# Performance work log

Hardware: AMD Instinct MI355X
Metric: run time of the kernel (lower is better)

## Reference

```python
import jax, jax.numpy as jnp
import numpy as np
from math import factorial, sqrt, pi

# ---- sizes ----
LMAX = 2; K = 32; NL = 4; NB = 8; PPOLY = 5.0; RMAX = 10.0
N = 1000; E = 8000; G = 4; XDIM = 26; MLP = 128
LS = (0, 1, 2)

# ---- real Clebsch-Gordan couplings (Racah formula + complex->real basis change) ----
def _cg_c(j1, m1, j2, m2, J, M):
    if M != m1 + m2 or J < abs(j1 - j2) or J > j1 + j2:
        return 0.0
    f = factorial
    pre = sqrt((2*J+1) * f(J+j1-j2) * f(J-j1+j2) * f(j1+j2-J) / f(j1+j2+J+1))
    pre *= sqrt(f(J+M)*f(J-M)*f(j1-m1)*f(j1+m1)*f(j2-m2)*f(j2+m2))
    s = 0.0
    for k in range(j1 + j2 - J + 1):
        d = (k, j1+j2-J-k, j1-m1-k, j2+m2-k, J-j2+m1+k, J-j1-m2+k)
        if min(d) < 0:
            continue
        den = 1.0
        for t in d:
            den *= f(t)
        s += (-1.0)**k / den
    return pre * s

def _u(l):
    U = np.zeros((2*l+1, 2*l+1), dtype=complex)
    for m in range(-l, l+1):
        i = m + l
        if m < 0:
            U[i, m+l] = 1j/sqrt(2); U[i, -m+l] = -1j*((-1.0)**m)/sqrt(2)
        elif m == 0:
            U[i, l] = 1.0
        else:
            U[i, -m+l] = 1/sqrt(2); U[i, m+l] = ((-1.0)**m)/sqrt(2)
    return U

def _real_cg(l1, l2, l3):
    Tc = np.zeros((2*l1+1, 2*l2+1, 2*l3+1), dtype=complex)
    for m1 in range(-l1, l1+1):
        for m2 in range(-l2, l2+1):
            Tc[m1+l1, m2+l2, :] = [_cg_c(l1, m1, l2, m2, l3, m3) for m3 in range(-l3, l3+1)]
    T = np.einsum('am,bn,co,mno->abc', _u(l1), _u(l2), _u(l3).conj(), Tc)
    T = T.real if np.abs(T.real).sum() >= np.abs(T.imag).sum() else T.imag
    return jnp.asarray(np.ascontiguousarray(T), dtype=jnp.float32)

CG = {}
for _l1 in LS:
    for _l2 in LS:
        for _l3 in LS:
            if abs(_l1-_l2) <= _l3 <= _l1+_l2 and (_l1+_l2+_l3) % 2 == 0:
                CG[(_l1, _l2, _l3)] = _real_cg(_l1, _l2, _l3)

CONVH = sorted(CG.keys())                 # 11 parity-allowed (l_in, l_sh, l_out) paths
CONV0 = [p for p in CONVH if p[0] == 0]   # 3 paths for first layer (Kx0e input)
NUMEL0 = len(CONV0) * K * K
NUMELH = len(CONVH) * K * K

PAIRS = {lo: [(l1, l2) for l1 in LS for l2 in LS if (l1, l2, lo) in CG] for lo in LS}
TRIPLES = {lo: [(l1, l2, L, l3) for L in LS for l3 in LS if (L, l3, lo) in CG
                for (l1, l2) in PAIRS[L]] for lo in LS}
MAXP2 = max(len(PAIRS[lo]) for lo in LS)     # 4
MAXP3 = max(len(TRIPLES[lo]) for lo in LS)   # 15
CG3 = {}
for _lo in LS:
    for (_a, _b, _L, _c) in TRIPLES[_lo]:
        CG3[(_a, _b, _L, _c, _lo)] = jnp.einsum('ijl,lmo->ijmo', CG[(_a, _b, _L)], CG[(_L, _c, _lo)])

# ---- geometry embeddings ----
def _sph(u):  # u: [E,3] unit vectors; component-normalized real SH, l=0..2
    x, y, z = u[:, 0], u[:, 1], u[:, 2]
    y0 = jnp.ones_like(x)[:, None]
    y1 = sqrt(3.0) * jnp.stack([y, z, x], -1)
    y2 = jnp.stack([sqrt(15.0)*x*y, sqrt(15.0)*y*z, sqrt(5.0)/2*(3*z*z - 1),
                    sqrt(15.0)*x*z, sqrt(15.0)/2*(x*x - y*y)], -1)
    return (y0, y1, y2)

def _radial(r):  # r: [E,1] -> [E,NB] Bessel basis * polynomial cutoff (p=5)
    n = jnp.arange(1, NB + 1, dtype=r.dtype)
    bess = sqrt(2.0 / RMAX) * jnp.sin(n * pi * r / RMAX) / r
    u = r / RMAX
    p = PPOLY
    cut = 1 - (p+1)*(p+2)/2 * u**5 + p*(p+2) * u**6 - p*(p+1)/2 * u**7
    return bess * jnp.where(u < 1.0, cut, 0.0)

# ---- tensor-product conv: per-edge MLP weights -> gather, CG tensor product, scatter-sum ----
def _conv(h, src, dst, sh, ef, w1, b1, w2, b2, paths):
    w = jax.nn.relu(ef @ w1 + b1) @ w2 + b2          # [E, weight_numel]
    nto = {lo: max(1, sum(1 for q in paths if q[2] == lo)) for lo in LS}
    msg = [jnp.zeros((src.shape[0], K, 2*lo + 1), w.dtype) for lo in LS]
    off = 0
    for (li, ls, lo) in paths:
        wp = w[:, off:off + K*K].reshape(-1, K, K); off += K * K
        t = jnp.einsum('eui,es,iso->euo', h[li][src], sh[ls], CG[(li, ls, lo)])
        msg[lo] = msg[lo] + jnp.einsum('euo,euv->evo', t, wp) / sqrt(K * nto[lo])
    return [jnp.zeros((N, K, 2*lo + 1), w.dtype).at[dst].add(msg[lo]) for lo in LS]

def _bn(h, w, b, eps=1e-5):  # e3nn-style irreps batch norm (training stats)
    out = []
    for l in LS:
        xl = h[l]
        if l == 0:
            mu = jnp.mean(xl, axis=0, keepdims=True)
            var = jnp.mean((xl - mu)**2, axis=0, keepdims=True)
            out.append((xl - mu) / jnp.sqrt(var + eps) * w[l][None, :, None] + b[None, :, None])
        else:
            n2 = jnp.mean(jnp.sum(xl * xl, -1), axis=0)  # [K]
            out.append(xl / jnp.sqrt(n2 + eps)[None, :, None] * w[l][None, :, None])
    return out

# ---- equivariant product-basis block (per-channel symmetric contractions, correlation 3) ----
def _prod(A, sc, w1, w2, w3, wlin, target_ls, use_sc):
    out = []
    for lo in target_ls:
        acc = w1[lo][None, :, None] * A[lo]
        for p, (l1, l2) in enumerate(PAIRS[lo]):
            t = jnp.einsum('nki,nkj,ijo->nko', A[l1], A[l2], CG[(l1, l2, lo)])
            acc = acc + w2[lo, p][None, :, None] * t
        for p, (l1, l2, L, l3) in enumerate(TRIPLES[lo]):
            t = jnp.einsum('nki,nkj,nkm,ijmo->nko', A[l1], A[l2], A[l3], CG3[(l1, l2, L, l3, lo)])
            acc = acc + w3[lo, p][None, :, None] * t
        y = jnp.einsum('nki,kv->nvi', acc, wlin[lo])
        if use_sc:
            y = y + sc[lo]
        out.append(y)
    return out

def _forward(x, pos, w_emb, b_emb, fc0_w1, fc0_b1, fc0_w2, fc0_b2,
             fcs_w1, fcs_b1, fcs_w2, fcs_b2, bn_w, bn_b, pw1, pw2, pw3, plin,
             edge_index, batch):
    src, dst = edge_index[0], edge_index[1]
    vec = pos[src] - pos[dst]
    r = jnp.maximum(jnp.linalg.norm(vec, axis=-1, keepdims=True), 1e-6)
    sh = _sph(vec / r)
    ef = _radial(r)
    h0 = x @ w_emb + b_emb
    h = [h0[:, :, None], jnp.zeros((N, K, 3), h0.dtype), jnp.zeros((N, K, 5), h0.dtype)]
    for i in range(NL):
        if i == 0:
            m = _conv(h, src, dst, sh, ef, fc0_w1, fc0_b1, fc0_w2, fc0_b2, CONV0)
        else:
            j = i - 1
            m = _conv(h, src, dst, sh, ef, fcs_w1[j], fcs_b1[j], fcs_w2[j], fcs_b2[j], CONVH)
        m = _bn(m, bn_w[i], bn_b[i])
        last = (i == NL - 1)
        h = _prod(m, h, pw1[i], pw2[i], pw3[i], plin[i],
                  target_ls=((0,) if last else LS), use_sc=(not last))
    node = h[0][:, :, 0]                                  # [N, K]
    graph = jax.ops.segment_sum(node, batch, num_segments=G)
    return node, graph

def setup_inputs() -> dict:
    key = jax.random.key(0)
    ks = jax.random.split(key, 16)
    rn = lambda k, sh, s: jax.random.normal(k, sh, dtype=jnp.float32) * s
    return dict(
        x=rn(ks[0], (N, XDIM), 1.0),
        pos=rn(ks[1], (N, 3), 3.0),
        edge_index=jax.random.randint(ks[2], (2, E), 0, N, dtype=jnp.int32),
        batch=jnp.sort(jax.random.randint(ks[3], (N,), 0, G, dtype=jnp.int32)),
        w_emb=rn(ks[4], (XDIM, K), 1.0/sqrt(XDIM)), b_emb=jnp.zeros((K,), jnp.float32),
        fc0_w1=rn(ks[5], (NB, MLP), 1.0/sqrt(NB)), fc0_b1=jnp.zeros((MLP,), jnp.float32),
        fc0_w2=rn(ks[6], (MLP, NUMEL0), 1.0/sqrt(MLP)), fc0_b2=jnp.zeros((NUMEL0,), jnp.float32),
        fcs_w1=rn(ks[7], (NL-1, NB, MLP), 1.0/sqrt(NB)), fcs_b1=jnp.zeros((NL-1, MLP), jnp.float32),
        fcs_w2=rn(ks[8], (NL-1, MLP, NUMELH), 1.0/sqrt(MLP)), fcs_b2=jnp.zeros((NL-1, NUMELH), jnp.float32),
        bn_w=jnp.ones((NL, 3, K), jnp.float32), bn_b=jnp.zeros((NL, K), jnp.float32),
        pw1=rn(ks[9], (NL, 3, K), 0.5),
        pw2=rn(ks[10], (NL, 3, MAXP2, K), 0.3),
        pw3=rn(ks[11], (NL, 3, MAXP3, K), 0.1),
        plin=rn(ks[12], (NL, 3, K, K), 1.0/sqrt(K)),
    )

def reference(x, pos, edge_index, batch, w_emb, b_emb, fc0_w1, fc0_b1, fc0_w2, fc0_b2,
              fcs_w1, fcs_b1, fcs_w2, fcs_b2, bn_w, bn_b, pw1, pw2, pw3, plin):
    return _forward(x, pos, w_emb, b_emb, fc0_w1, fc0_b1, fc0_w2, fc0_b2,
                    fcs_w1, fcs_b1, fcs_w2, fcs_b2, bn_w, bn_b, pw1, pw2, pw3, plin,
                    edge_index, batch)
```

## Files before the change

### kernel.cpp

```cpp
#include <hip/hip_runtime.h>
#include <hip/hip_bf16.h>
#include <math.h>

#define NE 8000
#define NN 1000
#define CAP 64
#define PLANE 256000

typedef unsigned short ushortt;
typedef __attribute__((ext_vector_type(8))) short short8;
typedef __attribute__((ext_vector_type(4))) float f32x4;

__device__ const int KEYL[11][3] = {{0,0,0},{0,1,1},{0,2,2},{1,0,1},{1,1,0},{1,1,2},{1,2,1},{2,0,2},{2,1,1},{2,2,0},{2,2,2}};
__device__ const int KEYOFF[12] = {0,1,10,35,44,53,98,143,168,213,238,363};

struct PathT { int li, ls, lo, cgoff, comp; };
__device__ const PathT PATHS[11] = {
 {0,0,0,  0, 0},{0,1,1,  1, 1},{0,2,2, 10, 4},{1,0,1, 35, 9},{1,1,0, 44,12},{1,1,2, 53,13},
 {1,2,1, 98,18},{2,0,2,143,21},{2,1,1,168,26},{2,2,0,213,29},{2,2,2,238,30}};

struct CPair { int l1,l2,cga; };
struct CTrip { int l1,l2,L,cga,l3,cgb; };
constexpr CPair cPR0[3]={{0,0,0},{1,1,44},{2,2,213}};
constexpr CPair cPR1[4]={{0,1,1},{1,0,35},{1,2,98},{2,1,168}};
constexpr CPair cPR2[4]={{0,2,10},{1,1,53},{2,0,143},{2,2,238}};
constexpr CTrip cTR0[11]={
  {0,0,0,0,0,0},{1,1,0,44,0,0},{2,2,0,213,0,0},
  {0,1,1,1,1,44},{1,0,1,35,1,44},{1,2,1,98,1,44},{2,1,1,168,1,44},
  {0,2,2,10,2,213},{1,1,2,53,2,213},{2,0,2,143,2,213},{2,2,2,238,2,213}};
constexpr CTrip cTR1[15]={
  {0,0,0,0,1,1},{1,1,0,44,1,1},{2,2,0,213,1,1},
  {0,1,1,1,0,35},{1,0,1,35,0,35},{1,2,1,98,0,35},{2,1,1,168,0,35},
  {0,1,1,1,2,98},{1,0,1,35,2,98},{1,2,1,98,2,98},{2,1,1,168,2,98},
  {0,2,2,10,1,168},{1,1,2,53,1,168},{2,0,2,143,1,168},{2,2,2,238,1,168}};
constexpr CTrip cTR2[15]={
  {0,0,0,0,2,10},{1,1,0,44,2,10},{2,2,0,213,2,10},
  {0,1,1,1,1,53},{1,0,1,35,1,53},{1,2,1,98,1,53},{2,1,1,168,1,53},
  {0,2,2,10,0,143},{1,1,2,53,0,143},{2,0,2,143,0,143},{2,2,2,238,0,143},
  {0,2,2,10,2,238},{1,1,2,53,2,238},{2,0,2,143,2,238},{2,2,2,238,2,238}};
constexpr CPair getPR(int lo,int p){ return lo==0?cPR0[p]:(lo==1?cPR1[p]:cPR2[p]); }
constexpr CTrip getTR(int lo,int p){ return lo==0?cTR0[p]:(lo==1?cTR1[p]:cTR2[p]); }
constexpr int cloff(int l){ return l==0?0:(l==1?1:4); }
constexpr int nPR(int lo){ return lo==0?3:4; }
constexpr int nTR(int lo){ return lo==0?11:15; }

template<int I> struct ic_t { static constexpr int v = I; };
template<int N, int I=0, typename F>
__device__ __forceinline__ void sfor(F&& f){
  if constexpr (I < N){ f(ic_t<I>{}); sfor<N, I+1>((F&&)f); }
}

__device__ __forceinline__ int loff_(int l){ return l==0?0:(l==1?1:4); }

__device__ __forceinline__ ushortt f2bf(float x){
  union { float f; unsigned int u; } a; a.f = x;
  unsigned int r = a.u + 0x7FFFu + ((a.u >> 16) & 1u);
  return (ushortt)(r >> 16);
}

__device__ __forceinline__ void gload_lds16(const void* g, void* lds){
  __builtin_amdgcn_global_load_lds((const __attribute__((address_space(1))) void*)g,
                                   (__attribute__((address_space(3))) void*)lds, 16, 0, 0);
}

__device__ double d_fact(int n){ double f=1.0; for(int i=2;i<=n;i++) f*=(double)i; return f; }

__device__ double d_cg(int j1,int m1,int j2,int m2,int J,int M){
  if (M != m1+m2 || J < abs(j1-j2) || J > j1+j2) return 0.0;
  double pre = sqrt((2.0*J+1.0)*d_fact(J+j1-j2)*d_fact(J-j1+j2)*d_fact(j1+j2-J)/d_fact(j1+j2+J+1));
  pre *= sqrt(d_fact(J+M)*d_fact(J-M)*d_fact(j1-m1)*d_fact(j1+m1)*d_fact(j2-m2)*d_fact(j2+m2));
  double s=0.0;
  for(int k=0;k<=j1+j2-J;k++){
    int d0=k, d1=j1+j2-J-k, d2=j1-m1-k, d3=j2+m2-k, d4=J-j2+m1+k, d5=J-j1-m2+k;
    if (d0<0||d1<0||d2<0||d3<0||d4<0||d5<0) continue;
    double den = d_fact(d0)*d_fact(d1)*d_fact(d2)*d_fact(d3)*d_fact(d4)*d_fact(d5);
    s += ((k&1)?-1.0:1.0)/den;
  }
  return pre*s;
}

__device__ void d_u(int l, int i, int j, double* re, double* im){
  int m = i - l;
  *re=0.0; *im=0.0;
  const double s2 = 0.70710678118654752440;
  double par = (m & 1) ? -1.0 : 1.0;
  if (m < 0){
    if (j == m + l)  *im += s2;
    if (j == -m + l) *im += -par*s2;
  } else if (m == 0){
    if (j == l) *re = 1.0;
  } else {
    if (j == -m + l) *re += s2;
    if (j == m + l)  *re += par*s2;
  }
}

__global__ __launch_bounds__(128) void kcg1(double* tmp){
  int key = blockIdx.x;
  int l1=KEYL[key][0], l2=KEYL[key][1], l3=KEYL[key][2];
  int n1=2*l1+1, n2=2*l2+1, n3=2*l3+1;
  int nel=n1*n2*n3;
  int t=threadIdx.x;
  if (t>=nel) return;
  int a=t/(n2*n3), b=(t/n3)%n2, c=t%n3;
  double sre=0.0, sim=0.0;
  for (int mi=0;mi<n1;mi++)
    for (int ni=0;ni<n2;ni++){
      int m3 = (mi-l1)+(ni-l2);
      int oi = m3 + l3;
      if (oi<0 || oi>=n3) continue;
      double tc = d_cg(l1,mi-l1,l2,ni-l2,l3,m3);
      if (tc==0.0) continue;
      double r1,i1,r2,i2,r3,i3;
      d_u(l1,a,mi,&r1,&i1);
      d_u(l2,b,ni,&r2,&i2);
      d_u(l3,c,oi,&r3,&i3);
      double rr = r1*r2 - i1*i2;
      double ri = r1*i2 + i1*r2;
      double fr = rr*r3 + ri*i3;
      double fi = ri*r3 - rr*i3;
      sre += fr*tc; sim += fi*tc;
    }
  tmp[(size_t)(KEYOFF[key]+t)*2]   = sre;
  tmp[(size_t)(KEYOFF[key]+t)*2+1] = sim;
}

__global__ __launch_bounds__(64) void kcg2(const double* tmp, float* cgf){
  int key=threadIdx.x;
  if (key>=11) return;
  int off=KEYOFF[key], n=KEYOFF[key+1]-off;
  double sre=0.0, sim=0.0;
  for (int i=0;i<n;i++){ sre += fabs(tmp[(size_t)(off+i)*2]); sim += fabs(tmp[(size_t)(off+i)*2+1]); }
  bool takeRe = (sre >= sim);
  for (int i=0;i<n;i++) cgf[off+i] = (float)(takeRe ? tmp[(size_t)(off+i)*2] : tmp[(size_t)(off+i)*2+1]);
}

__global__ __launch_bounds__(256) void kgeom(const float* __restrict__ pos, const int* __restrict__ ei,
                                             float* __restrict__ shb, float* __restrict__ efb){
  int e = blockIdx.x*256+threadIdx.x;
  if (e>=NE) return;
  int s=ei[e], d=ei[NE+e];
  float vx=pos[s*3]-pos[d*3], vy=pos[s*3+1]-pos[d*3+1], vz=pos[s*3+2]-pos[d*3+2];
  float r = sqrtf(vx*vx+vy*vy+vz*vz);
  r = fmaxf(r, 1e-6f);
  float inv = 1.0f/r;
  float x=vx*inv, y=vy*inv, z=vz*inv;
  float* sh = shb + (size_t)e*9;
  const float s3=1.7320508075688772f, s15=3.872983346207417f, s5h=1.118033988749895f, s15h=1.9364916731037085f;
  sh[0]=1.0f;
  sh[1]=s3*y; sh[2]=s3*z; sh[3]=s3*x;
  sh[4]=s15*x*y; sh[5]=s15*y*z; sh[6]=s5h*(3.0f*z*z-1.0f); sh[7]=s15*x*z; sh[8]=s15h*(x*x-y*y);
  float u=r*0.1f;
  float cut=0.0f;
  if (u<1.0f){ float u2=u*u; float u5=u2*u2*u; cut = 1.0f - 21.0f*u5 + 35.0f*u5*u - 15.0f*u5*u2; }
  const float c0 = 0.4472135954999579f;
  const float PIF = 3.14159265358979323846f;
  float* ef = efb + (size_t)e*8;
  for (int j=0;j<8;j++)
    ef[j] = c0*sinf((float)(j+1)*PIF*r*0.1f)*inv*cut;
}

__global__ __launch_bounds__(256) void kembed(const float* __restrict__ x, const float* __restrict__ wemb,
                                              const float* __restrict__ bemb, float* __restrict__ h){
  int idx = blockIdx.x*256+threadIdx.x;
  if (idx>=NN*32) return;
  int n=idx>>5, k=idx&31;
  float a=bemb[k];
  for (int d=0;d<26;d++) a += x[n*26+d]*wemb[d*32+k];
  float* hp = h + (size_t)n*288 + k*9;
  hp[0]=a;
  #pragma unroll
  for (int c=1;c<9;c++) hp[c]=0.0f;
}

__global__ __launch_bounds__(256) void ktrans(const float* __restrict__ fc0_w2, const float* __restrict__ fcs_w2,
                                              ushortt* __restrict__ w2t0, ushortt* __restrict__ w2tH){
  int layer = blockIdx.z;
  int numel = (layer==0) ? 3072 : 11264;
  int c0 = blockIdx.x*32;
  if (c0 >= numel) return;
  const float* src = (layer==0) ? fc0_w2 : fcs_w2 + (size_t)(layer-1)*128*11264;
  ushortt* dst = (layer==0) ? w2t0 : w2tH + (size_t)(layer-1)*11264*128;
  int k0 = blockIdx.y*32;
  __shared__ float tile[32][33];
  int t = threadIdx.x;
  #pragma unroll
  for (int it=0; it<4; it++){
    int r = (t>>5) + it*8;
    tile[r][t&31] = src[(size_t)(k0+r)*numel + c0 + (t&31)];
  }
  __syncthreads();
  #pragma unroll
  for (int it=0; it<4; it++){
    int c = (t>>5) + it*8;
    int k = t&31;
    dst[(size_t)(c0+c)*128 + k0 + k] = f2bf(tile[k][c]);
  }
}

__global__ __launch_bounds__(256) void khid2(const float* __restrict__ efb, const float* __restrict__ w1,
                                             const float* __restrict__ b1, ushortt* __restrict__ hidbf){
  int idx = blockIdx.x*256+threadIdx.x;
  if (idx >= NE*16) return;
  int e = idx>>4, q = idx&15;
  int m0 = q*8;
  float efr[8];
  const float* ef = efb + (size_t)e*8;
  #pragma unroll
  for (int j=0;j<8;j++) efr[j]=ef[j];
  ushortt out8[8];
  #pragma unroll
  for (int mm=0;mm<8;mm++){
    int m = m0+mm;
    float a = b1[m];
    #pragma unroll
    for (int j=0;j<8;j++) a = fmaf(efr[j], w1[j*128+m], a);
    out8[mm] = f2bf(a>0.0f?a:0.0f);
  }
  *(short8*)(hidbf + (size_t)e*128 + m0) = *(const short8*)out8;
}

template<int NO>
__global__ __launch_bounds__(256, (NO==1?3:2)) void kmsg5(
    const float* __restrict__ hc, const float* __restrict__ shb,
    const ushortt* __restrict__ hidbf, const ushortt* __restrict__ w2t,
    const float* __restrict__ b2, const float* __restrict__ cg,
    const int* __restrict__ src, float* __restrict__ msgp, int plist){
  int p = (plist >> (blockIdx.y*8)) & 0xFF;
  int e0 = blockIdx.x*64;
  int li=PATHS[p].li, ls=PATHS[p].ls;
  int n1=2*li+1, ns=2*ls+1;
  int lioff=loff_(li), lsoff=loff_(ls);
  int cgoff=PATHS[p].cgoff;
  int comp=PATHS[p].comp;

  __shared__ __align__(16) ushortt sB[2][64*128];
  __shared__ __align__(16) float   sT[NO*2048];
  __shared__ __align__(16) float   sB2[1024];
  __shared__ int     sSRC[64];
  float* ov  = (float*)&sB[1][0];
  float* sCP = ov;
  float* sSH = ov + 1600;

  int t = threadIdx.x;
  int w = t>>6, l = t&63;

  #pragma unroll
  for (int q=0;q<4;q++){
    int R0 = w*16 + q*4;
    int row = R0 + (l>>4);
    int ks = ((l&15)*8) ^ ((row&7)<<3);
    gload_lds16(w2t + (size_t)(p*1024 + row)*128 + ks, &sB[0][R0*128]);
  }
  short8 av[4];
  {
    const ushortt* ap = hidbf + (size_t)(e0 + w*16 + (l&15))*128 + (l>>4)*8;
    #pragma unroll
    for (int kk=0;kk<4;kk++) av[kk] = *(const short8*)(ap + kk*32);
  }
  #pragma unroll
  for (int q=0;q<4;q++) sB2[t + q*256] = b2[p*1024 + t + q*256];
  if (t < 64) sSRC[t] = src[e0+t];
  for (int idx=t; idx<64*9; idx+=256) sSH[idx] = shb[(size_t)e0*9 + idx];
  __syncthreads();

  for (int idx=t; idx<64*n1*NO; idx+=256){
    int e=idx/(n1*NO), r=idx%(n1*NO), i=r/NO, o=r%NO;
    float a=0.0f;
    for (int s=0;s<ns;s++) a += cg[cgoff + (i*ns+s)*NO+o]*sSH[e*9 + lsoff + s];
    sCP[e*25 + i*NO + o]=a;
  }
  __syncthreads();

  for (int idx=t; idx<64*32; idx+=256){
    int e = idx&63, u = idx>>6;
    const float* hp = hc + (size_t)sSRC[e]*288 + u*9 + lioff;
    float hv[5];
    #pragma unroll
    for (int i=0;i<5;i++) hv[i] = hp[i];
    #pragma unroll
    for (int o=0;o<NO;o++){
      float a=0.0f;
      #pragma unroll
      for (int i=0;i<5;i++) if (i<n1) a = fmaf(hv[i], sCP[e*25 + i*NO + o], a);
      sT[(u*NO+o)*64 + e] = a;
    }
  }
  __syncthreads();

  float macc[4][2][NO];
  #pragma unroll
  for (int r=0;r<4;r++)
    #pragma unroll
    for (int vh=0;vh<2;vh++)
      #pragma unroll
      for (int o=0;o<NO;o++) macc[r][vh][o]=0.0f;

  int e_idx = w*16 + (l>>4)*4;

  for (int c=0;c<16;c++){
    int buf = c&1;
    if (c<15){
      #pragma unroll
      for (int q=0;q<4;q++){
        int R0 = w*16 + q*4;
        int row = R0 + (l>>4);
        int ks = ((l&15)*8) ^ ((row&7)<<3);
        gload_lds16(w2t + (size_t)(p*1024 + (c+1)*64 + row)*128 + ks, &sB[buf^1][R0*128]);
      }
    }
    f32x4 acc[4];
    #pragma unroll
    for (int fn=0;fn<4;fn++)
      #pragma unroll
      for (int r=0;r<4;r++) acc[fn][r]=0.0f;
    __builtin_amdgcn_s_setprio(1);
    #pragma unroll
    for (int kk=0; kk<4; kk++){
      #pragma unroll
      for (int fn=0; fn<4; fn++){
        int brow = fn*16 + (l&15);
        int kb = (kk*32 + (l>>4)*8) ^ ((brow&7)<<3);
        short8 bv = *(const short8*)&sB[buf][brow*128 + kb];
        acc[fn] = __builtin_amdgcn_mfma_f32_16x16x32_bf16(av[kk], bv, acc[fn], 0,0,0);
      }
    }
    __builtin_amdgcn_s_setprio(0);
    #pragma unroll
    for (int uu=0;uu<2;uu++){
      int ug = c*2 + uu;
      f32x4 tv[NO];
      #pragma unroll
      for (int o=0;o<NO;o++) tv[o] = *(const f32x4*)&sT[(ug*NO+o)*64 + e_idx];
      #pragma unroll
      for (int vh=0;vh<2;vh++){
        int fn = uu*2+vh;
        float b2v = sB2[c*64 + fn*16 + (l&15)];
        #pragma unroll
        for (int r=0;r<4;r++){
          float Cv = acc[fn][r] + b2v;
          #pragma unroll
          for (int o=0;o<NO;o++) macc[r][vh][o] = fmaf(Cv, tv[o][r], macc[r][vh][o]);
        }
      }
    }
    __syncthreads();
  }

  float* sW = sT;
  #pragma unroll
  for (int r=0;r<4;r++){
    int e = e_idx + r;
    #pragma unroll
    for (int vh=0;vh<2;vh++){
      int v = vh*16 + (l&15);
      int g = v>>2;
      int addr = e*32 + (((g ^ (e&7)))<<2) + (v&3);
      #pragma unroll
      for (int o=0;o<NO;o++)
        sW[o*2048 + addr] = macc[r][vh][o];
    }
  }
  __syncthreads();
  for (int j=t; j<NO*512; j+=256){
    int o = j>>9, q = j&511;
    int e = q>>3, gl = q&7;
    f32x4 vv = *(const f32x4*)&sW[o*2048 + e*32 + ((gl^(e&7))<<2)];
    *(f32x4*)(msgp + (size_t)(comp+o)*PLANE + (size_t)e0*32 + q*4) = vv;
  }
}

__global__ __launch_bounds__(320) void kbuild(const int* __restrict__ dst, int* __restrict__ cnt, int* __restrict__ lst){
  int n = blockIdx.x;
  int t = threadIdx.x;
  __shared__ int s_dstl[NE];
  __shared__ int s_cnt[321];
  for (int idx=t; idx<NE; idx+=320) s_dstl[idx]=dst[idx];
  __syncthreads();
  const int per = NE/320;
  int start=t*per, end=start+per;
  int c=0;
  for (int e=start;e<end;++e) if (s_dstl[e]==n) c++;
  s_cnt[t+1]=c;
  if (t==0) s_cnt[0]=0;
  __syncthreads();
  if (t==0){ for (int i=1;i<=320;i++) s_cnt[i]+=s_cnt[i-1]; }
  __syncthreads();
  int pos = s_cnt[t];
  for (int e=start;e<end;++e) if (s_dstl[e]==n){ if (pos<CAP) lst[n*CAP+pos]=e; pos++; }
  if (t==0){ int M=s_cnt[320]; cnt[n]=(M<CAP)?M:CAP; }
}

__global__ __launch_bounds__(320) void kgather2(const float* __restrict__ msgp, const int* __restrict__ cnt,
                                                const int* __restrict__ lst, float* __restrict__ mbuf, int full){
  int n = blockIdx.x;
  int t = threadIdx.x;
  if (t >= 288) return;
  int M = cnt[n];
  int jc = t>>5, k = t&31;
  float acc=0.0f;
  if (full){
    int pl0,pl1,pl2,pl3,np;
    if (jc==0){ pl0=0; pl1=12; pl2=29; pl3=0; np=3; }
    else if (jc<4){ int o=jc-1; pl0=1+o; pl1=9+o; pl2=18+o; pl3=26+o; np=4; }
    else { int o=jc-4; pl0=4+o; pl1=13+o; pl2=21+o; pl3=30+o; np=4; }
    for (int m=0;m<M;++m){
      int e = lst[n*CAP+m];
      int base = e*32 + k;
      float a = msgp[(size_t)pl0*PLANE + base] + msgp[(size_t)pl1*PLANE + base] + msgp[(size_t)pl2*PLANE + base];
      if (np==4) a += msgp[(size_t)pl3*PLANE + base];
      acc += a;
    }
  } else {
    for (int m=0;m<M;++m){
      int e = lst[n*CAP+m];
      acc += msgp[(size_t)jc*PLANE + e*32 + k];
    }
  }
  float norm = full ? (jc==0 ? 0.10206207261596577f : 0.08838834764831845f) : 0.17677669529663687f;
  mbuf[(size_t)n*288 + k*9 + jc] = acc*norm;
}

__global__ __launch_bounds__(256) void kbn(const float* __restrict__ mbuf, float* __restrict__ stats){
  int k = blockIdx.x, t = threadIdx.x;
  float s0=0,sq0=0,sq1=0,sq2=0;
  for (int n=t;n<NN;n+=256){
    const float* mp = mbuf + (size_t)n*288 + k*9;
    float v0=mp[0]; s0+=v0; sq0+=v0*v0;
    float a=mp[1],b=mp[2],c=mp[3]; sq1+=a*a+b*b+c*c;
    float d=mp[4],e=mp[5],f=mp[6],g=mp[7],h=mp[8]; sq2+=d*d+e*e+f*f+g*g+h*h;
  }
  __shared__ float r[4][256];
  r[0][t]=s0; r[1][t]=sq0; r[2][t]=sq1; r[3][t]=sq2;
  __syncthreads();
  for (int s=128;s>0;s>>=1){
    if (t<s){ r[0][t]+=r[0][t+s]; r[1][t]+=r[1][t+s]; r[2][t]+=r[2][t+s]; r[3][t]+=r[3][t+s]; }
    __syncthreads();
  }
  if (t==0){
    float mu = r[0][0]/(float)NN;
    float var = r[1][0]/(float)NN - mu*mu;
    stats[k]      = mu;
    stats[32+k]   = rsqrtf(var + 1e-5f);
    stats[64+k]   = rsqrtf(r[2][0]/(float)NN + 1e-5f);
    stats[96+k]   = rsqrtf(r[3][0]/(float)NN + 1e-5f);
  }
}

template<int CGA,int NA,int AO,int NB,int BO,int NO>
__device__ __forceinline__ void c2u(const float* __restrict__ cg, const float (&A)[9], const float (&B)[9], float (&out)[5]){
  #pragma unroll
  for (int o=0;o<NO;o++) out[o]=0.0f;
  #pragma unroll
  for (int i=0;i<NA;i++){
    #pragma unroll
    for (int j=0;j<NB;j++){
      float ab=A[AO+i]*B[BO+j];
      #pragma unroll
      for (int o=0;o<NO;o++) out[o]=fmaf(ab, cg[CGA+(i*NB+j)*NO+o], out[o]);
    }
  }
}
template<int CGA,int NA,int NB,int BO,int NO>
__device__ __forceinline__ void c2u5(const float* __restrict__ cg, const float (&Bb)[5], const float (&A)[9], float (&out)[5]){
  #pragma unroll
  for (int o=0;o<NO;o++) out[o]=0.0f;
  #pragma unroll
  for (int i=0;i<NA;i++){
    #pragma unroll
    for (int j=0;j<NB;j++){
      float ab=Bb[i]*A[BO+j];
      #pragma unroll
      for (int o=0;o<NO;o++) out[o]=fmaf(ab, cg[CGA+(i*NB+j)*NO+o], out[o]);
    }
  }
}

template<int LO>
__device__ __forceinline__ void do_lo(const float* __restrict__ cg, const float (&A)[9], float (&L)[9],
                                      const float* __restrict__ w1, const float* __restrict__ w2,
                                      const float* __restrict__ w3, int k){
  constexpr int NO=2*LO+1, AO=cloff(LO);
  float acc[5];
  float wc = w1[LO*32+k];
  #pragma unroll
  for (int o=0;o<NO;o++) acc[o]=wc*A[AO+o];
  sfor<nPR(LO)>([&](auto pc){
    constexpr int p = decltype(pc)::v;
    constexpr CPair P = getPR(LO,p);
    float tt[5];
    c2u<P.cga, 2*P.l1+1, cloff(P.l1), 2*P.l2+1, cloff(P.l2), NO>(cg, A, A, tt);
    float w = w2[(LO*4+p)*32+k];
    #pragma unroll
    for (int o=0;o<NO;o++) acc[o]=fmaf(w, tt[o], acc[o]);
  });
  sfor<nTR(LO)>([&](auto pc){
    constexpr int p = decltype(pc)::v;
    constexpr CTrip T = getTR(LO,p);
    constexpr int NL=2*T.L+1;
    float bb[5];
    c2u<T.cga, 2*T.l1+1, cloff(T.l1), 2*T.l2+1, cloff(T.l2), NL>(cg, A, A, bb);
    float tt[5];
    c2u5<T.cgb, NL, 2*T.l3+1, cloff(T.l3), NO>(cg, bb, A, tt);
    float w = w3[(LO*15+p)*32+k];
    #pragma unroll
    for (int o=0;o<NO;o++) acc[o]=fmaf(w, tt[o], acc[o]);
  });
  #pragma unroll
  for (int o=0;o<NO;o++) L[AO+o]=acc[o];
}

template<int LAST>
__global__ __launch_bounds__(256) void kprod3(const float* __restrict__ mbuf, const float* __restrict__ stats,
    const float* __restrict__ hc, float* __restrict__ hn,
    const float* __restrict__ bnw, const float* __restrict__ bnb,
    const float* __restrict__ w1, const float* __restrict__ w2, const float* __restrict__ w3,
    const float* __restrict__ plin, const float* __restrict__ cg, float* __restrict__ nodeout){
  int t = threadIdx.x;
  int nl = t>>5, k = t&31;
  int n = blockIdx.x*8 + nl;
  __shared__ float sL[8][32][9];
  float A[9], L[9];
  #pragma unroll
  for (int j=0;j<9;j++) L[j]=0.0f;
  const float* mp = mbuf + (size_t)n*288 + k*9;
  {
    float a0 = (mp[0]-stats[k])*stats[32+k]*bnw[k] + bnb[k];
    float f1 = stats[64+k]*bnw[32+k];
    float f2 = stats[96+k]*bnw[64+k];
    A[0]=a0;
    A[1]=mp[1]*f1; A[2]=mp[2]*f1; A[3]=mp[3]*f1;
    #pragma unroll
    for (int c=0;c<5;c++) A[4+c]=mp[4+c]*f2;
  }
  do_lo<0>(cg, A, L, w1, w2, w3, k);
  if constexpr (!LAST){
    do_lo<1>(cg, A, L, w1, w2, w3, k);
    do_lo<2>(cg, A, L, w1, w2, w3, k);
  }
  #pragma unroll
  for (int j=0;j<9;j++) sL[nl][k][j]=L[j];
  __syncthreads();

  if constexpr (!LAST){
    for (int idx=t; idx<8*288; idx+=256){
      int n2 = idx/288;
      int r  = idx%288;
      int jc = r>>5, v = r&31;
      int lo = (jc==0)?0:((jc<4)?1:2);
      float y=0.0f;
      const float* pl = plin + lo*1024 + v;
      for (int kk=0;kk<32;kk++)
        y = fmaf(sL[n2][kk][jc], pl[kk*32], y);
      int ng = blockIdx.x*8 + n2;
      y += hc[(size_t)ng*288 + v*9 + jc];
      hn[(size_t)ng*288 + v*9 + jc] = y;
    }
  } else {
    int n2 = t>>5, v = t&31;
    float y=0.0f;
    const float* pl = plin + v;
    for (int kk=0;kk<32;kk++)
      y = fmaf(sL[n2][kk][0], pl[kk*32], y);
    nodeout[(size_t)(blockIdx.x*8+n2)*32 + v] = y;
  }
}

__global__ __launch_bounds__(256) void kgraphA(const float* __restrict__ nodeout, const int* __restrict__ batch,
                                               float* __restrict__ partial){
  int b = blockIdx.x;
  int t = threadIdx.x;
  __shared__ float sv[8][32];
  __shared__ int   sg[8];
  int nl = t>>5, k = t&31;
  int n = b*8 + nl;
  sv[nl][k] = nodeout[(size_t)n*32 + k];
  if (k==0) sg[nl] = batch[n];
  __syncthreads();
  if (t < 128){
    int g = t>>5, kk = t&31;
    float acc=0.0f;
    #pragma unroll
    for (int j=0;j<8;j++) if (sg[j]==g) acc += sv[j][kk];
    partial[((size_t)b*4 + g)*32 + kk] = acc;
  }
}

__global__ __launch_bounds__(128) void kgraphB(const float* __restrict__ partial, float* __restrict__ gout){
  int t = threadIdx.x;
  int g = t>>5, k = t&31;
  float acc=0.0f;
  for (int b=0;b<125;b++) acc += partial[((size_t)b*4 + g)*32 + k];
  gout[g*32 + k] = acc;
}

extern "C" void kernel_launch(void* const* d_in, const int* in_sizes, int n_in,
                              void* d_out, int out_size, void* d_ws, size_t ws_size,
                              hipStream_t stream) {
  const float* x      = (const float*)d_in[0];
  const float* pos    = (const float*)d_in[1];
  const int*   ei     = (const int*)d_in[2];
  const int*   batch  = (const int*)d_in[3];
  const float* w_emb  = (const float*)d_in[4];
  const float* b_emb  = (const float*)d_in[5];
  const float* fc0_w1 = (const float*)d_in[6];
  const float* fc0_b1 = (const float*)d_in[7];
  const float* fc0_w2 = (const float*)d_in[8];
  const float* fc0_b2 = (const float*)d_in[9];
  const float* fcs_w1 = (const float*)d_in[10];
  const float* fcs_b1 = (const float*)d_in[11];
  const float* fcs_w2 = (const float*)d_in[12];
  const float* fcs_b2 = (const float*)d_in[13];
  const float* bn_w   = (const float*)d_in[14];
  const float* bn_b   = (const float*)d_in[15];
  const float* pw1    = (const float*)d_in[16];
  const float* pw2    = (const float*)d_in[17];
  const float* pw3    = (const float*)d_in[18];
  const float* plin   = (const float*)d_in[19];

  double* cgtmp = (double*)d_ws;
  float*  F     = (float*)d_ws;
  float*  cgf   = F + 1456;
  float*  shb   = F + 1824;
  float*  efb   = F + 73824;
  float*  hA    = F + 137824;
  float*  hB    = F + 425824;
  float*  mbuf  = F + 713824;
  float*  stats = F + 1001824;
  float*  msgb  = F + 1001952;
  ushortt* hidbf = (ushortt*)(F + 9961952);
  ushortt* w2t0  = (ushortt*)(F + 10473952);
  ushortt* w2tH  = (ushortt*)(F + 10670560);
  int* csr_cnt = (int*)(F + 12833248);
  int* csr_lst = csr_cnt + 1024;
  float* partial = F + 12900000;

  float* nodeout = (float*)d_out;
  float* gout    = (float*)d_out + NN*32;

  kcg1<<<11,128,0,stream>>>(cgtmp);
  kcg2<<<1,64,0,stream>>>(cgtmp, cgf);
  kgeom<<<(NE+255)/256,256,0,stream>>>(pos, ei, shb, efb);
  kembed<<<(NN*32+255)/256,256,0,stream>>>(x, w_emb, b_emb, hA);
  ktrans<<<dim3(352,4,4),256,0,stream>>>(fc0_w2, fcs_w2, w2t0, w2tH);
  kbuild<<<NN,320,0,stream>>>(ei+NE, csr_cnt, csr_lst);

  float* hc = hA;
  float* hn = hB;
  for (int i=0;i<4;i++){
    const float *w1,*b1,*b2; const ushortt* w2t; int full;
    if (i==0){ w1=fc0_w1; b1=fc0_b1; w2t=w2t0; b2=fc0_b2; full=0; }
    else {
      int j=i-1;
      w1=fcs_w1 + (size_t)j*1024;
      b1=fcs_b1 + (size_t)j*128;
      w2t=w2tH + (size_t)j*11264*128;
      b2=fcs_b2 + (size_t)j*11264;
      full=1;
    }
    khid2<<<(NE*16+255)/256,256,0,stream>>>(efb, w1, b1, hidbf);
    if (full){
      kmsg5<1><<<dim3(125,3),256,0,stream>>>(hc, shb, hidbf, w2t, b2, cgf, ei, msgb, 0 | (4<<8) | (9<<16));
      kmsg5<3><<<dim3(125,4),256,0,stream>>>(hc, shb, hidbf, w2t, b2, cgf, ei, msgb, 1 | (3<<8) | (6<<16) | (8<<24));
      kmsg5<5><<<dim3(125,4),256,0,stream>>>(hc, shb, hidbf, w2t, b2, cgf, ei, msgb, 2 | (5<<8) | (7<<16) | (10<<24));
    } else {
      kmsg5<1><<<dim3(125,1),256,0,stream>>>(hc, shb, hidbf, w2t, b2, cgf, ei, msgb, 0);
      kmsg5<3><<<dim3(125,1),256,0,stream>>>(hc, shb, hidbf, w2t, b2, cgf, ei, msgb, 1);
      kmsg5<5><<<dim3(125,1),256,0,stream>>>(hc, shb, hidbf, w2t, b2, cgf, ei, msgb, 2);
    }
    kgather2<<<NN,320,0,stream>>>(msgb, csr_cnt, csr_lst, mbuf, full);
    kbn<<<32,256,0,stream>>>(mbuf, stats);
    int last = (i==3);
    const float* bw = bn_w + (size_t)i*96;
    const float* bb = bn_b + (size_t)i*32;
    const float* p1 = pw1 + (size_t)i*96;
    const float* p2 = pw2 + (size_t)i*384;
    const float* p3 = pw3 + (size_t)i*1440;
    const float* pl = plin + (size_t)i*3072;
    if (!last)
      kprod3<0><<<NN/8,256,0,stream>>>(mbuf, stats, hc, hn, bw, bb, p1, p2, p3, pl, cgf, nodeout);
    else
      kprod3<1><<<NN/8,256,0,stream>>>(mbuf, stats, hc, hn, bw, bb, p1, p2, p3, pl, cgf, nodeout);
    float* tmp=hc; hc=hn; hn=tmp;
  }
  kgraphA<<<125,256,0,stream>>>(nodeout, batch, partial);
  kgraphB<<<1,128,0,stream>>>(partial, gout);
}
```

Before: 584.7 us.

## Prefetch two weight tiles ahead in message kernel with explicit vmcnt waits

The message kernel now issues global-to-LDS loads for both W2 tiles up front. The main loop uses explicit s_waitcnt vmcnt and raw s_barrier instead of __syncthreads, and the load for tile c+2 is issued after the compute on tile c. The SH and CG scratch arrays move out of the second B buffer into their own shared arrays, so that buffer can be filled early. This aims to hide global load latency behind the MFMA work, at the cost of extra LDS use, which may lower occupancy, and fragile hand-written wait counts.

```diff
diff --git a/kernel.cpp b/kernel.cpp
--- a/kernel.cpp
+++ b/kernel.cpp
@@ -221,7 +221,7 @@
 }
 
 template<int NO>
-__global__ __launch_bounds__(256, (NO==1?3:2)) void kmsg5(
+__global__ __launch_bounds__(256, (NO==1?3:2)) void kmsg10(
     const float* __restrict__ hc, const float* __restrict__ shb,
     const ushortt* __restrict__ hidbf, const ushortt* __restrict__ w2t,
     const float* __restrict__ b2, const float* __restrict__ cg,
@@ -239,8 +239,11 @@
   __shared__ __align__(16) float   sB2[1024];
   __shared__ int     sSRC[64];
   float* ov  = (float*)&sB[1][0];
-  float* sCP = ov;
-  float* sSH = ov + 1600;
+  __shared__ __align__(16) float sCPb[64*25];
+  __shared__ __align__(16) float sSHb[64*9];
+  float* sCP = sCPb;
+  float* sSH = sSHb;
+  (void)ov;
 
   int t = threadIdx.x;
   int w = t>>6, l = t&63;
@@ -252,6 +255,13 @@
     int ks = ((l&15)*8) ^ ((row&7)<<3);
     gload_lds16(w2t + (size_t)(p*1024 + row)*128 + ks, &sB[0][R0*128]);
   }
+  #pragma unroll
+  for (int q=0;q<4;q++){
+    int R0 = w*16 + q*4;
+    int row = R0 + (l>>4);
+    int ks = ((l&15)*8) ^ ((row&7)<<3);
+    gload_lds16(w2t + (size_t)(p*1024 + 64 + row)*128 + ks, &sB[1][R0*128]);
+  }
   short8 av[4];
   {
     const ushortt* ap = hidbf + (size_t)(e0 + w*16 + (l&15))*128 + (l>>4)*8;
@@ -300,15 +310,9 @@
 
   for (int c=0;c<16;c++){
     int buf = c&1;
-    if (c<15){
-      #pragma unroll
-      for (int q=0;q<4;q++){
-        int R0 = w*16 + q*4;
-        int row = R0 + (l>>4);
-        int ks = ((l&15)*8) ^ ((row&7)<<3);
-        gload_lds16(w2t + (size_t)(p*1024 + (c+1)*64 + row)*128 + ks, &sB[buf^1][R0*128]);
-      }
-    }
+    if (c<15) { asm volatile("s_waitcnt vmcnt(4)" ::: "memory"); }
+    else      { asm volatile("s_waitcnt vmcnt(0)" ::: "memory"); }
+    asm volatile("s_barrier" ::: "memory");
     f32x4 acc[4];
     #pragma unroll
     for (int fn=0;fn<4;fn++)
@@ -344,7 +348,16 @@
         }
       }
     }
-    __syncthreads();
+    asm volatile("s_barrier" ::: "memory");
+    if (c+2<16){
+      #pragma unroll
+      for (int q=0;q<4;q++){
+        int R0 = w*16 + q*4;
+        int row = R0 + (l>>4);
+        int ks = ((l&15)*8) ^ ((row&7)<<3);
+        gload_lds16(w2t + (size_t)(p*1024 + (c+2)*64 + row)*128 + ks, &sB[buf][R0*128]);
+      }
+    }
   }
 
   float* sW = sT;
@@ -660,13 +673,13 @@
     }
     khid2<<<(NE*16+255)/256,256,0,stream>>>(efb, w1, b1, hidbf);
     if (full){
-      kmsg5<1><<<dim3(125,3),256,0,stream>>>(hc, shb, hidbf, w2t, b2, cgf, ei, msgb, 0 | (4<<8) | (9<<16));
-      kmsg5<3><<<dim3(125,4),256,0,stream>>>(hc, shb, hidbf, w2t, b2, cgf, ei, msgb, 1 | (3<<8) | (6<<16) | (8<<24));
-      kmsg5<5><<<dim3(125,4),256,0,stream>>>(hc, shb, hidbf, w2t, b2, cgf, ei, msgb, 2 | (5<<8) | (7<<16) | (10<<24));
+      kmsg10<1><<<dim3(125,3),256,0,stream>>>(hc, shb, hidbf, w2t, b2, cgf, ei, msgb, 0 | (4<<8) | (9<<16));
+      kmsg10<3><<<dim3(125,4),256,0,stream>>>(hc, shb, hidbf, w2t, b2, cgf, ei, msgb, 1 | (3<<8) | (6<<16) | (8<<24));
+      kmsg10<5><<<dim3(125,4),256,0,stream>>>(hc, shb, hidbf, w2t, b2, cgf, ei, msgb, 2 | (5<<8) | (7<<16) | (10<<24));
     } else {
-      kmsg5<1><<<dim3(125,1),256,0,stream>>>(hc, shb, hidbf, w2t, b2, cgf, ei, msgb, 0);
-      kmsg5<3><<<dim3(125,1),256,0,stream>>>(hc, shb, hidbf, w2t, b2, cgf, ei, msgb, 1);
-      kmsg5<5><<<dim3(125,1),256,0,stream>>>(hc, shb, hidbf, w2t, b2, cgf, ei, msgb, 2);
+      kmsg10<1><<<dim3(125,1),256,0,stream>>>(hc, shb, hidbf, w2t, b2, cgf, ei, msgb, 0);
+      kmsg10<3><<<dim3(125,1),256,0,stream>>>(hc, shb, hidbf, w2t, b2, cgf, ei, msgb, 1);
+      kmsg10<5><<<dim3(125,1),256,0,stream>>>(hc, shb, hidbf, w2t, b2, cgf, ei, msgb, 2);
     }
     kgather2<<<NN,320,0,stream>>>(msgb, csr_cnt, csr_lst, mbuf, full);
     kbn<<<32,256,0,stream>>>(mbuf, stats);
```

New measurement: 602.1 us. 3.0% more time.
